# Kernel optimization log

Hardware: AMD Instinct MI355X
Metric: run time of the kernel (lower is better)

The kernel has to match this reference:

```python
import jax, jax.numpy as jnp
import numpy as np

EPS = 1e-12  # F.normalize default eps


def setup_inputs() -> dict:
    key = jax.random.key(0)
    k1, k2 = jax.random.split(key)
    E, N, B, T, Fdim, K = 2, 512, 64, 12, 2, 64
    supports = jax.random.uniform(k1, (E, N, N), dtype=jnp.float32)
    inputs = jax.random.normal(k2, (B, T, N, Fdim), dtype=jnp.float32)
    bias = jnp.ones((E, K), dtype=jnp.float32)  # init.ones_
    # torch.svd at __init__: A = u @ diag(s) @ v^T, truncated to node_dim
    u_np, s_np, vh_np = np.linalg.svd(np.asarray(supports), full_matrices=False)
    u = jnp.asarray(u_np[..., :K])                      # [E, N, K]
    s = jnp.asarray(s_np[..., :K])                      # [E, K]
    v = jnp.asarray(np.swapaxes(vh_np, -1, -2)[..., :K])  # [E, N, K]
    return {"supports": supports, "u": u, "s": s, "v": v, "bias": bias, "inputs": inputs}


def _pairwise_dist(x):
    # x: [B, N, T] L2-normalized rows; returns [B, N, N] Euclidean distances
    sq = jnp.sum(x * x, axis=-1)                      # [B, N]
    inner = jnp.einsum('bnt,bmt->bnm', x, x)          # [B, N, N]
    d2 = jnp.maximum(sq[:, :, None] + sq[:, None, :] - 2.0 * inner, 0.0)
    # safe sqrt (zero on the diagonal, matching torch.cdist)
    pos = d2 > 0
    return jnp.where(pos, jnp.sqrt(jnp.where(pos, d2, 1.0)), 0.0)


def reference(supports, u, s, v, bias, inputs):
    # SAdaptor: low-rank SVD reconstruction with softplus-scaled singular values
    s_scaled = s * jax.nn.softplus(bias)              # [E, K]
    adaptive = jnp.einsum('enk,ek,emk->enm', u, s_scaled, v)  # [E, N, N]
    sup = supports + adaptive                         # [E, N, N]

    # TAdaptor: exp(-cdist) of L2-normalized node histories (dropout: eval mode)
    x = jnp.transpose(inputs[..., 0], (0, 2, 1))      # [B, N, T]
    nrm = jnp.sqrt(jnp.sum(x * x, axis=-1, keepdims=True))
    nodes = x / jnp.maximum(nrm, EPS)                 # F.normalize(p=2)
    dynamic = jnp.exp(-_pairwise_dist(nodes))         # [B, N, N]

    out = sup[:, None, :, :] * (dynamic[None] + 1.0)  # [E, B, N, N]
    out = jax.nn.relu(out)
    # F.normalize(p=1, dim=-1); out >= 0 so |out| == out
    return out / jnp.maximum(jnp.sum(out, axis=-1, keepdims=True), EPS)
```

## Files before the change

### kernel.cpp

```cpp
#include <hip/hip_runtime.h>

#define E 2
#define N 512
#define B 64
#define T 12
#define K 64
#define NBR 8
#define RPB 32

template<int CTRL, int RM>
__device__ __forceinline__ float dpp_add(float x) {
    int y = __builtin_amdgcn_update_dpp(0, __float_as_int(x), CTRL, RM, 0xf, true);
    return x + __int_as_float(y);
}
__device__ __forceinline__ float wave_sum64(float x) {
    x = dpp_add<0x111, 0xf>(x);
    x = dpp_add<0x112, 0xf>(x);
    x = dpp_add<0x114, 0xf>(x);
    x = dpp_add<0x118, 0xf>(x);
    x = dpp_add<0x142, 0xa>(x);
    x = dpp_add<0x143, 0xc>(x);
    return __int_as_float(__builtin_amdgcn_readlane(__float_as_int(x), 63));
}

__global__ __launch_bounds__(512)
void k_prep(const float* __restrict__ supports, const float* __restrict__ uu,
            const float* __restrict__ ss, const float* __restrict__ vv,
            const float* __restrict__ bias, const float* __restrict__ inp,
            float* __restrict__ sup, float* __restrict__ nodes,
            float* __restrict__ nodesT) {
    const int blk = blockIdx.x, tid = threadIdx.x;
    if (blk < 256) {
        const int e = blk >> 7;
        const int n0 = (blk & 127) * 4;
        __shared__ float uls[4][K];
        if (tid < 4 * K) {
            const int j = tid >> 6, k = tid & 63;
            float bb = bias[e * K + k];
            float sp_ = (bb > 0.f) ? (bb + log1pf(expf(-bb))) : log1pf(expf(bb));
            uls[j][k] = uu[(size_t)(e * N + n0 + j) * K + k] * ss[e * K + k] * sp_;
        }
        __syncthreads();
        const int m = tid;
        const float4* vp = reinterpret_cast<const float4*>(vv + (size_t)(e * N + m) * K);
        float accs[4] = {0.f, 0.f, 0.f, 0.f};
#pragma unroll
        for (int i = 0; i < 16; ++i) {
            float4 q = vp[i];
#pragma unroll
            for (int j = 0; j < 4; ++j) {
                const float* w = &uls[j][i * 4];
                accs[j] += w[0] * q.x + w[1] * q.y + w[2] * q.z + w[3] * q.w;
            }
        }
#pragma unroll
        for (int j = 0; j < 4; ++j) {
            const size_t o = (size_t)(e * N + n0 + j) * N + m;
            sup[o] = accs[j] + supports[o];
        }
    } else {
        const int b = blk - 256;
        const int n = tid;
        float x[T];
        float sq = 0.f;
#pragma unroll
        for (int t = 0; t < T; ++t) {
            float xv = inp[((size_t)(b * T + t) * N + n) * 2];
            x[t] = xv;
            sq += xv * xv;
        }
        float inv = 1.f / fmaxf(sqrtf(sq), 1e-12f);
#pragma unroll
        for (int t = 0; t < T; ++t) {
            float xv = x[t] * inv;
            nodes[((size_t)(b * N) + n) * T + t] = xv;
            nodesT[((size_t)(b * T) + t) * N + n] = xv;
        }
    }
}

__global__ __launch_bounds__(256)
void k_main(const float* __restrict__ sup, const float* __restrict__ nodes,
            const float* __restrict__ nodesT, float* __restrict__ out) {
    const int bi = blockIdx.x;
    const int b = bi >> 4;
    const int wave = __builtin_amdgcn_readfirstlane((int)threadIdx.x >> 6);
    const int lane = threadIdx.x & 63;
    const int n0 = (bi & 15) * RPB + wave * NBR;
    const int m0 = lane * 8;

    float x[T][8];
#pragma unroll
    for (int t = 0; t < T; ++t) {
        const float* cp = nodesT + ((size_t)(b * T) + t) * N + m0;
        float4 c0 = *reinterpret_cast<const float4*>(cp);
        float4 c1 = *reinterpret_cast<const float4*>(cp + 4);
        x[t][0] = c0.x; x[t][1] = c0.y; x[t][2] = c0.z; x[t][3] = c0.w;
        x[t][4] = c1.x; x[t][5] = c1.y; x[t][6] = c1.z; x[t][7] = c1.w;
    }

#pragma unroll
    for (int j = 0; j < NBR; ++j) {
        const int n = n0 + j;
        const float* ap = nodes + ((size_t)(b * N) + n) * T;
        float4 a0 = *reinterpret_cast<const float4*>(ap);
        float4 a1 = *reinterpret_cast<const float4*>(ap + 4);
        float4 a2 = *reinterpret_cast<const float4*>(ap + 8);
        float a[T] = {a0.x, a0.y, a0.z, a0.w, a1.x, a1.y, a1.z, a1.w,
                      a2.x, a2.y, a2.z, a2.w};

        const float* s0p = sup + (size_t)n * N + m0;
        const float* s1p = s0p + (size_t)N * N;
        float4 sA = *reinterpret_cast<const float4*>(s0p);
        float4 sB = *reinterpret_cast<const float4*>(s0p + 4);
        float4 sC = *reinterpret_cast<const float4*>(s1p);
        float4 sD = *reinterpret_cast<const float4*>(s1p + 4);
        float sp0[8] = {sA.x, sA.y, sA.z, sA.w, sB.x, sB.y, sB.z, sB.w};
        float sp1[8] = {sC.x, sC.y, sC.z, sC.w, sD.x, sD.y, sD.z, sD.w};

        float v0[8], v1[8];
        float p0 = 0.f, p1 = 0.f;
#pragma unroll
        for (int k = 0; k < 8; ++k) {
            float dot = 0.f;
#pragma unroll
            for (int t = 0; t < T; ++t) dot = fmaf(x[t][k], a[t], dot);
            float d2 = fmaxf(2.f - 2.f * dot, 0.f);
            float f = __expf(-sqrtf(d2)) + 1.f;
            v0[k] = fmaxf(sp0[k] * f, 0.f);
            v1[k] = fmaxf(sp1[k] * f, 0.f);
            p0 += v0[k];
            p1 += v1[k];
        }
        float inv0 = 1.f / fmaxf(wave_sum64(p0), 1e-12f);
        float inv1 = 1.f / fmaxf(wave_sum64(p1), 1e-12f);

        float* o0 = out + ((size_t)(b * N) + n) * N + m0;
        float* o1 = o0 + (size_t)B * N * N;
        *reinterpret_cast<float4*>(o0) =
            make_float4(v0[0] * inv0, v0[1] * inv0, v0[2] * inv0, v0[3] * inv0);
        *reinterpret_cast<float4*>(o0 + 4) =
            make_float4(v0[4] * inv0, v0[5] * inv0, v0[6] * inv0, v0[7] * inv0);
        *reinterpret_cast<float4*>(o1) =
            make_float4(v1[0] * inv1, v1[1] * inv1, v1[2] * inv1, v1[3] * inv1);
        *reinterpret_cast<float4*>(o1 + 4) =
            make_float4(v1[4] * inv1, v1[5] * inv1, v1[6] * inv1, v1[7] * inv1);
    }
}

extern "C" void kernel_launch(void* const* d_in, const int* in_sizes, int n_in,
                              void* d_out, int out_size, void* d_ws, size_t ws_size,
                              hipStream_t stream) {
    const float* supports = (const float*)d_in[0];
    const float* uu       = (const float*)d_in[1];
    const float* ss       = (const float*)d_in[2];
    const float* vv       = (const float*)d_in[3];
    const float* bias     = (const float*)d_in[4];
    const float* inp      = (const float*)d_in[5];
    float* out = (float*)d_out;

    float* sup    = (float*)d_ws;
    float* nodes  = sup + (size_t)E * N * N;
    float* nodesT = nodes + (size_t)B * N * T;

    k_prep<<<256 + B, 512, 0, stream>>>(supports, uu, ss, vv, bias, inp,
                                        sup, nodes, nodesT);
    k_main<<<B * (N / RPB), 256, 0, stream>>>(sup, nodes, nodesT, out);
}
```

Before: 167.1 us.

## Stage row node vectors in LDS and compute 8x8 dot tile up front

Each block now loads the 32 rows' transposed node vectors into shared memory. Each wave then computes an 8x8 register tile of dot products by streaming over T, instead of holding all T×8 column values in registers and reloading each row's node vector from global memory. The dot computation is hoisted out of the per-row loop, and a launch-bounds occupancy hint is added. This trades x-register pressure for a 64-float accumulator tile and adds one block barrier. The kernel remains dominated by output stores.

```diff
diff --git a/kernel.cpp b/kernel.cpp
--- a/kernel.cpp
+++ b/kernel.cpp
@@ -5,8 +5,6 @@
 #define B 64
 #define T 12
 #define K 64
-#define NBR 8
-#define RPB 32
 
 template<int CTRL, int RM>
 __device__ __forceinline__ float dpp_add(float x) {
@@ -79,36 +77,49 @@
     }
 }
 
-__global__ __launch_bounds__(256)
-void k_main(const float* __restrict__ sup, const float* __restrict__ nodes,
-            const float* __restrict__ nodesT, float* __restrict__ out) {
+__global__ __launch_bounds__(256, 4)
+void k_main(const float* __restrict__ sup, const float* __restrict__ nodesT,
+            float* __restrict__ out) {
     const int bi = blockIdx.x;
     const int b = bi >> 4;
+    const int n0blk = (bi & 15) * 32;
     const int wave = __builtin_amdgcn_readfirstlane((int)threadIdx.x >> 6);
     const int lane = threadIdx.x & 63;
-    const int n0 = (bi & 15) * RPB + wave * NBR;
     const int m0 = lane * 8;
 
-    float x[T][8];
+    __shared__ float aT[T][32];
+    for (int idx = threadIdx.x; idx < T * 32; idx += 256) {
+        const int t = idx >> 5, r = idx & 31;
+        aT[t][r] = nodesT[((size_t)(b * T) + t) * N + n0blk + r];
+    }
+    __syncthreads();
+
+    float dot[8][8];
 #pragma unroll
+    for (int j = 0; j < 8; ++j)
+#pragma unroll
+        for (int k = 0; k < 8; ++k) dot[j][k] = 0.f;
+
+    const float* xbase = nodesT + (size_t)(b * T) * N + m0;
+#pragma unroll 2
     for (int t = 0; t < T; ++t) {
-        const float* cp = nodesT + ((size_t)(b * T) + t) * N + m0;
-        float4 c0 = *reinterpret_cast<const float4*>(cp);
-        float4 c1 = *reinterpret_cast<const float4*>(cp + 4);
-        x[t][0] = c0.x; x[t][1] = c0.y; x[t][2] = c0.z; x[t][3] = c0.w;
-        x[t][4] = c1.x; x[t][5] = c1.y; x[t][6] = c1.z; x[t][7] = c1.w;
+        float4 x4a = *reinterpret_cast<const float4*>(xbase + (size_t)t * N);
+        float4 x4b = *reinterpret_cast<const float4*>(xbase + (size_t)t * N + 4);
+        const float* ap = &aT[t][wave * 8];
+        float4 a4a = *reinterpret_cast<const float4*>(ap);
+        float4 a4b = *reinterpret_cast<const float4*>(ap + 4);
+        const float xs[8] = {x4a.x, x4a.y, x4a.z, x4a.w, x4b.x, x4b.y, x4b.z, x4b.w};
+        const float as[8] = {a4a.x, a4a.y, a4a.z, a4a.w, a4b.x, a4b.y, a4b.z, a4b.w};
+#pragma unroll
+        for (int j = 0; j < 8; ++j)
+#pragma unroll
+            for (int k = 0; k < 8; ++k)
+                dot[j][k] = fmaf(xs[k], as[j], dot[j][k]);
     }
 
 #pragma unroll
-    for (int j = 0; j < NBR; ++j) {
-        const int n = n0 + j;
-        const float* ap = nodes + ((size_t)(b * N) + n) * T;
-        float4 a0 = *reinterpret_cast<const float4*>(ap);
-        float4 a1 = *reinterpret_cast<const float4*>(ap + 4);
-        float4 a2 = *reinterpret_cast<const float4*>(ap + 8);
-        float a[T] = {a0.x, a0.y, a0.z, a0.w, a1.x, a1.y, a1.z, a1.w,
-                      a2.x, a2.y, a2.z, a2.w};
-
+    for (int j = 0; j < 8; ++j) {
+        const int n = n0blk + wave * 8 + j;
         const float* s0p = sup + (size_t)n * N + m0;
         const float* s1p = s0p + (size_t)N * N;
         float4 sA = *reinterpret_cast<const float4*>(s0p);
@@ -122,10 +133,7 @@
         float p0 = 0.f, p1 = 0.f;
 #pragma unroll
         for (int k = 0; k < 8; ++k) {
-            float dot = 0.f;
-#pragma unroll
-            for (int t = 0; t < T; ++t) dot = fmaf(x[t][k], a[t], dot);
-            float d2 = fmaxf(2.f - 2.f * dot, 0.f);
+            float d2 = fmaxf(2.f - 2.f * dot[j][k], 0.f);
             float f = __expf(-sqrtf(d2)) + 1.f;
             v0[k] = fmaxf(sp0[k] * f, 0.f);
             v1[k] = fmaxf(sp1[k] * f, 0.f);
@@ -165,5 +173,5 @@
 
     k_prep<<<256 + B, 512, 0, stream>>>(supports, uu, ss, vv, bias, inp,
                                         sup, nodes, nodesT);
-    k_main<<<B * (N / RPB), 256, 0, stream>>>(sup, nodes, nodesT, out);
+    k_main<<<B * (N / 32), 256, 0, stream>>>(sup, nodesT, out);
 }
```

Measured after the change: 164.3 us. About the same (-1.7%).
